# Kernel tuning notes

Hardware: AMD Instinct MI355X
Metric: run time of the kernel (lower is better)

Reference implementation:

```python
import jax, jax.numpy as jnp
import numpy as np

B, N, C = 8, 4096, 768
H = 12            # num_heads
W = 16            # window_size
S = int(N ** 0.5) # 64, token grid side
HD = C // H       # head_dim = 64
WINDOWS = (S // W) ** 2  # 16
NW = W * W               # 256 tokens per window
SCALE = HD ** -0.5


def _window_perm():
    # same ordering as the torch loop: row-major over window blocks,
    # row-major within each window
    idxs = np.arange(N).reshape(S // W, W, S // W, W)
    perm = idxs.transpose(0, 2, 1, 3).reshape(-1)
    inv_perm = np.argsort(perm)
    return jnp.asarray(perm), jnp.asarray(inv_perm)


def setup_inputs() -> dict:
    key = jax.random.key(0)
    kx, kq, kp, kb = jax.random.split(key, 4)
    x = jax.random.normal(kx, (B, N, C), dtype=jnp.float32)
    # torch nn.Linear weights: [out, in]; qkv_bias=False
    qkv_w = jax.random.normal(kq, (3 * C, C), dtype=jnp.float32) * (C ** -0.5)
    proj_w = jax.random.normal(kp, (C, C), dtype=jnp.float32) * (C ** -0.5)
    proj_b = jax.random.normal(kb, (C,), dtype=jnp.float32) * 0.02
    return {"x": x, "qkv_w": qkv_w, "proj_w": proj_w, "proj_b": proj_b}


def reference(x, qkv_w, proj_w, proj_b):
    perm, inv_perm = _window_perm()
    xp = x[:, perm]                                   # [B, N, C] window-ordered
    qkv = xp @ qkv_w.T                                # [B, N, 3C]
    qkv = qkv.reshape(B, WINDOWS, NW, 3, H, HD)
    qkv = jnp.transpose(qkv, (3, 0, 1, 4, 2, 5))      # [3, B, Wn, H, NW, HD]
    q, k, v = qkv[0], qkv[1], qkv[2]
    attn = jnp.einsum('bwhnd,bwhmd->bwhnm', q, k) * SCALE
    attn = jax.nn.softmax(attn, axis=-1)
    out = jnp.einsum('bwhnm,bwhmd->bwhnd', attn, v)   # [B, Wn, H, NW, HD]
    out = jnp.transpose(out, (0, 1, 3, 2, 4)).reshape(B, N, C)
    out = out[:, inv_perm]                            # scatter back to grid order
    return out @ proj_w.T + proj_b
```

## Files before the change

### kernel.cpp

```cpp
#include <hip/hip_runtime.h>
#include <hip/hip_bf16.h>


using short8  = __attribute__((ext_vector_type(8))) short;
using short4v = __attribute__((ext_vector_type(4))) short;
using floatx4 = __attribute__((ext_vector_type(4))) float;

#define B_    8
#define N_    4096
#define C_    768
#define H_    12
#define HD_   64
#define NW_   256
#define SCALE_ 0.125f
#define QKV_PLANE ((size_t)25165824)

__device__ __forceinline__ float bf2f(unsigned short u) {
  union { unsigned int i; float f; } c; c.i = ((unsigned int)u) << 16; return c.f;
}
__device__ __forceinline__ unsigned short f2bf(float f) {
  unsigned int u = __float_as_uint(f);
  u += 0x7fffu + ((u >> 16) & 1u);
  return (unsigned short)(u >> 16);
}
__device__ __forceinline__ short4v f4bf(floatx4 f) {
  short4v s;
  s[0] = (short)f2bf(f[0]); s[1] = (short)f2bf(f[1]);
  s[2] = (short)f2bf(f[2]); s[3] = (short)f2bf(f[3]);
  return s;
}
__device__ __forceinline__ int perm_n(int w, int t) {
  int rb = w >> 2, cb = w & 3, ri = t >> 4, ci = t & 15;
  return ((rb << 4) + ri) * 64 + (cb << 4) + ci;
}
__device__ __forceinline__ void glds16(const unsigned short* g, short* l) {
  __builtin_amdgcn_global_load_lds(
      (const __attribute__((address_space(1))) unsigned int*)g,
      (__attribute__((address_space(3))) unsigned int*)l, 16, 0, 0);
}

__global__ __launch_bounds__(192) void conv_x(
    const float* __restrict__ x, unsigned short* __restrict__ xb) {
  int row = blockIdx.x;
  int b = row >> 12, p = row & 4095;
  int n = perm_n(p >> 8, p & 255);
  const float* src = x + ((size_t)(b << 12) + (size_t)n) * C_;
  unsigned short* dst = xb + (size_t)row * C_;
  int c = threadIdx.x << 2;
  *(short4v*)(dst + c) = f4bf(*(const floatx4*)(src + c));
}

__global__ __launch_bounds__(192) void conv_w(
    const float* __restrict__ qw, const float* __restrict__ pw,
    unsigned short* __restrict__ wq, unsigned short* __restrict__ wp) {
  int row = blockIdx.x;
  const float* src; unsigned short* dst;
  if (row < 2304) { src = qw + (size_t)row * C_; dst = wq + (size_t)row * C_; }
  else { src = pw + (size_t)(row - 2304) * C_; dst = wp + (size_t)(row - 2304) * C_; }
  int c = threadIdx.x << 2;
  *(short4v*)(dst + c) = f4bf(*(const floatx4*)(src + c));
}

#define LPA 0
#define LPB 16384
#define LQA 32768
#define LQB 49152

#define STAGE8(gp, ldsbase, ksk) {                                             \
    int kc_ = (ksk) < C_ ? (ksk) : 0;                                          \
    glds16((gp) + (size_t)arow * C_ + kc_ + (sgran << 3),                      \
           L + (ldsbase) + tid * 8);                                           \
    glds16((gp) + (size_t)(arow + 64) * C_ + kc_ + (sgran << 3),               \
           L + (ldsbase) + 4096 + tid * 8);                                    \
  }

#define PH8(q, AB, BB, LOADB, STG_STMT, WV) {                                  \
    if (LOADB) {                                                               \
      _Pragma("unroll") for (int n = 0; n < 4; n++)                            \
        _Pragma("unroll") for (int kk = 0; kk < 2; kk++)                       \
          bq[n][kk] = *(const short8*)&L[(BB) + rdB + n * 1024 +               \
                                          (((kk * 4 + quad) ^ swq) << 3)];     \
    }                                                                          \
    short8 a0k0 = *(const short8*)&L[(AB) + rdA + (2*(q))*1024 +               \
                                      (((quad) ^ swq) << 3)];                  \
    short8 a0k1 = *(const short8*)&L[(AB) + rdA + (2*(q))*1024 +               \
                                      (((4 + quad) ^ swq) << 3)];              \
    short8 a1k0 = *(const short8*)&L[(AB) + rdA + (2*(q)+1)*1024 +             \
                                      (((quad) ^ swq) << 3)];                  \
    short8 a1k1 = *(const short8*)&L[(AB) + rdA + (2*(q)+1)*1024 +             \
                                      (((4 + quad) ^ swq) << 3)];              \
    STG_STMT;                                                                  \
    asm volatile("s_barrier" ::: "memory");                                    \
    asm volatile("s_waitcnt lgkmcnt(0)" ::: "memory");                         \
    __builtin_amdgcn_sched_barrier(0);                                         \
    __builtin_amdgcn_s_setprio(1);                                             \
    _Pragma("unroll") for (int n = 0; n < 4; n++) {                            \
      acc[2*(q)][n]   = __builtin_amdgcn_mfma_f32_16x16x32_bf16(               \
          a0k0, bq[n][0], acc[2*(q)][n], 0, 0, 0);                             \
      acc[2*(q)+1][n] = __builtin_amdgcn_mfma_f32_16x16x32_bf16(               \
          a1k0, bq[n][0], acc[2*(q)+1][n], 0, 0, 0);                           \
      acc[2*(q)][n]   = __builtin_amdgcn_mfma_f32_16x16x32_bf16(               \
          a0k1, bq[n][1], acc[2*(q)][n], 0, 0, 0);                             \
      acc[2*(q)+1][n] = __builtin_amdgcn_mfma_f32_16x16x32_bf16(               \
          a1k1, bq[n][1], acc[2*(q)+1][n], 0, 0, 0);                           \
    }                                                                          \
    __builtin_amdgcn_s_setprio(0);                                             \
    if (WV) { asm volatile("s_waitcnt vmcnt(4)" ::: "memory"); }               \
    asm volatile("s_barrier" ::: "memory");                                    \
  }

#define GEMM8_CORE(Aptr, Bptr)                                                 \
  __shared__ short L[65536];                                                   \
  const int tid  = threadIdx.x;                                                \
  const int bm   = blockIdx.x;                                                 \
  const int bn   = blockIdx.y;                                                 \
  const int wave = tid >> 6, lane = tid & 63;                                  \
  const int wm   = wave >> 2, wn = wave & 3;                                   \
  const int l15  = lane & 15, quad = lane >> 4;                                \
  const int swq  = l15 & 7;                                                    \
  const int sgran = (tid & 7) ^ ((tid >> 3) & 7);                              \
  const int arow  = tid >> 3;                                                  \
  const unsigned short* gA = (Aptr) + (size_t)(bm * 256) * C_;                 \
  const unsigned short* gB = (Bptr) + (size_t)(bn * 256) * C_;                 \
  const unsigned short* gA1 = gA + (size_t)128 * C_;                           \
  const unsigned short* gB1 = gB + (size_t)128 * C_;                           \
  const int rdA = wm * 8192 + l15 * 64;                                        \
  const int rdB = (wn >> 1) * 8192 + ((wn & 1) * 64 + l15) * 64;               \
  floatx4 acc[8][4];                                                           \
  short8 bq[4][2];                                                             \
  _Pragma("unroll") for (int i = 0; i < 8; i++)                                \
      _Pragma("unroll") for (int j = 0; j < 4; j++)                            \
          acc[i][j] = {0.f, 0.f, 0.f, 0.f};                                    \
                           \
  STAGE8(gA,  LPA,        0); STAGE8(gA1, LPA + 8192, 0);                      \
  STAGE8(gB,  LPB,        0); STAGE8(gB1, LPB + 8192, 0);                      \
  STAGE8(gB,  LQB,       64); STAGE8(gB1, LQB + 8192, 64);                     \
  asm volatile("s_waitcnt vmcnt(4)" ::: "memory");                             \
  asm volatile("s_barrier" ::: "memory");                                      \
  for (int it = 0; it < 6; it++) {                                             \
    const int t  = it * 2;                                                     \
    const int kA1 = (t + 1) * 64;                                              \
    const int kN2 = (t + 2) * 64;                                              \
    const int kN3 = (t + 3) * 64;                                              \
    PH8(0, LPA, LPB, 1, STAGE8(gA,  LQA,        kA1), 0)                       \
    PH8(1, LPA, LPB, 0, STAGE8(gA1, LQA + 8192, kA1), 0)                       \
    PH8(2, LPA, LPB, 0, STAGE8(gB,  LPB,        kN2), 0)                       \
    PH8(3, LPA, LPB, 0, STAGE8(gB1, LPB + 8192, kN2), 1)                       \
    PH8(0, LQA, LQB, 1, STAGE8(gA,  LPA,        kN2), 0)                       \
    PH8(1, LQA, LQB, 0, STAGE8(gA1, LPA + 8192, kN2), 0)                       \
    PH8(2, LQA, LQB, 0, STAGE8(gB,  LQB,        kN3), 0)                       \
    PH8(3, LQA, LQB, 0, STAGE8(gB1, LQB + 8192, kN3), 1)                       \
  }

__global__ __launch_bounds__(512, 2) void qkv_gemm_bf8(
    const unsigned short* __restrict__ a,
    const unsigned short* __restrict__ w,
    unsigned short* __restrict__ qkv) {
  GEMM8_CORE(a, w)
  const int which = bn / 3;
  const int jbase = (bn - which * 3) * 256;
  unsigned short* dst = qkv + (size_t)which * QKV_PLANE;
#pragma unroll
  for (int mi = 0; mi < 8; mi++) {
#pragma unroll
    for (int r = 0; r < 4; r++) {
      int mg = bm * 256 + wm * 128 + mi * 16 + quad * 4 + r;
      int b = mg >> 12, p = mg & 4095;
      int wdx = p >> 8, tt = p & 255;
      size_t base = (size_t)((b * 16 + wdx) * 12) * (NW_ * HD_) + (size_t)tt * HD_;
#pragma unroll
      for (int ni = 0; ni < 4; ni++) {
        int jj = jbase + wn * 64 + ni * 16 + l15;
        int h = jj >> 6, d = jj & 63;
        dst[base + (size_t)h * (NW_ * HD_) + d] = f2bf(acc[mi][ni][r]);
      }
    }
  }
  asm volatile("s_waitcnt vmcnt(0)" ::: "memory");
}

__global__ __launch_bounds__(512, 2) void proj_gemm_bf8(
    const unsigned short* __restrict__ a,
    const unsigned short* __restrict__ w,
    const float* __restrict__ bias,
    float* __restrict__ out) {
  GEMM8_CORE(a, w)
#pragma unroll
  for (int mi = 0; mi < 8; mi++) {
#pragma unroll
    for (int r = 0; r < 4; r++) {
      int mg = bm * 256 + wm * 128 + mi * 16 + quad * 4 + r;
      size_t rowb = (size_t)mg * C_;
#pragma unroll
      for (int ni = 0; ni < 4; ni++) {
        int jj = bn * 256 + wn * 64 + ni * 16 + l15;
        out[rowb + jj] = acc[mi][ni][r] + bias[jj];
      }
    }
  }
  asm volatile("s_waitcnt vmcnt(0)" ::: "memory");
}

__global__ __launch_bounds__(512, 2) void attn_mfma(
    const unsigned short* __restrict__ qkv,
    unsigned short* __restrict__ attn_out) {
  const int bwh = blockIdx.x;
  const int tid = threadIdx.x;
  const int wv = tid >> 6, lane = tid & 63;
  const int l15 = lane & 15, quad = lane >> 4;
  const size_t off = (size_t)bwh * (NW_ * HD_);
  const unsigned short* qb = qkv + off;
  const unsigned short* kb = qkv + QKV_PLANE + off;
  const unsigned short* vb = qkv + 2 * QKV_PLANE + off;

  __shared__ short Ks[64 * 72];
  __shared__ short Vt[64 * 72];
  __shared__ short Ps[8][16 * 72];

  short8 bq[2][2];
#pragma unroll
  for (int c = 0; c < 2; c++) {
    int mc = wv + 8 * c;
#pragma unroll
    for (int kc = 0; kc < 2; kc++)
      bq[c][kc] = *(const short8*)(qb + (mc * 16 + l15) * 64 + kc * 32 + quad * 8);
  }

  floatx4 O[2][4];
#pragma unroll
  for (int c = 0; c < 2; c++)
#pragma unroll
    for (int dt = 0; dt < 4; dt++) O[c][dt] = {0.f, 0.f, 0.f, 0.f};
  float m_run[2] = {-1e30f, -1e30f};
  float l_run[2] = {0.f, 0.f};

  const int sr = tid >> 3;
  const int sc = (tid & 7) << 3;

  for (int t = 0; t < 4; t++) {
    __syncthreads();
    {
      short8 kk8 = *(const short8*)(kb + (t * 64 + sr) * 64 + sc);
      *(short8*)&Ks[sr * 72 + sc] = kk8;
      short8 vv8 = *(const short8*)(vb + (t * 64 + sr) * 64 + sc);
#pragma unroll
      for (int j = 0; j < 8; j++) Vt[(sc + j) * 72 + sr] = vv8[j];
    }
    __syncthreads();

#pragma unroll
    for (int c = 0; c < 2; c++) {
      floatx4 st[4];
#pragma unroll
      for (int nt = 0; nt < 4; nt++) {
        short8 ak0 = *(const short8*)&Ks[(nt * 16 + l15) * 72 + quad * 8];
        short8 ak1 = *(const short8*)&Ks[(nt * 16 + l15) * 72 + 32 + quad * 8];
        floatx4 z = {0.f, 0.f, 0.f, 0.f};
        z = __builtin_amdgcn_mfma_f32_16x16x32_bf16(ak0, bq[c][0], z, 0, 0, 0);
        z = __builtin_amdgcn_mfma_f32_16x16x32_bf16(ak1, bq[c][1], z, 0, 0, 0);
        st[nt] = z;
      }
      float s[16];
      float cmax = -1e30f;
#pragma unroll
      for (int nt = 0; nt < 4; nt++)
#pragma unroll
        for (int r = 0; r < 4; r++) {
          float v = st[nt][r] * SCALE_;
          s[nt * 4 + r] = v;
          cmax = fmaxf(cmax, v);
        }
      cmax = fmaxf(cmax, __shfl_xor(cmax, 16));
      cmax = fmaxf(cmax, __shfl_xor(cmax, 32));
      float nm = fmaxf(m_run[c], cmax);
      float alpha = __expf(m_run[c] - nm);
      m_run[c] = nm;
      float psum = 0.f;
#pragma unroll
      for (int j = 0; j < 16; j++) {
        float p = __expf(s[j] - nm);
        s[j] = p;
        psum += p;
      }
      psum += __shfl_xor(psum, 16);
      psum += __shfl_xor(psum, 32);
      l_run[c] = l_run[c] * alpha + psum;
#pragma unroll
      for (int nt = 0; nt < 4; nt++) {
        short4v pv;
        pv[0] = (short)f2bf(s[nt * 4 + 0]);
        pv[1] = (short)f2bf(s[nt * 4 + 1]);
        pv[2] = (short)f2bf(s[nt * 4 + 2]);
        pv[3] = (short)f2bf(s[nt * 4 + 3]);
        *(short4v*)&Ps[wv][l15 * 72 + nt * 16 + quad * 4] = pv;
      }
      float ar[4];
#pragma unroll
      for (int r = 0; r < 4; r++) ar[r] = __shfl(alpha, quad * 4 + r);
#pragma unroll
      for (int dt = 0; dt < 4; dt++)
#pragma unroll
        for (int r = 0; r < 4; r++) O[c][dt][r] *= ar[r];
#pragma unroll
      for (int kc = 0; kc < 2; kc++) {
        short8 ap = *(const short8*)&Ps[wv][l15 * 72 + kc * 32 + quad * 8];
#pragma unroll
        for (int dt = 0; dt < 4; dt++) {
          short8 bv = *(const short8*)&Vt[(dt * 16 + l15) * 72 + kc * 32 + quad * 8];
          O[c][dt] = __builtin_amdgcn_mfma_f32_16x16x32_bf16(ap, bv, O[c][dt], 0, 0, 0);
        }
      }
    }
  }

  int h = bwh % 12, bw = bwh / 12;
  int b = bw >> 4, wdx = bw & 15;
#pragma unroll
  for (int c = 0; c < 2; c++) {
    float linv = 1.f / l_run[c];
    float lr[4];
#pragma unroll
    for (int r = 0; r < 4; r++) lr[r] = __shfl(linv, quad * 4 + r);
    int mc = wv + 8 * c;
#pragma unroll
    for (int r = 0; r < 4; r++) {
      int q = mc * 16 + quad * 4 + r;
      int n = perm_n(wdx, q);
      unsigned short* op = attn_out + ((size_t)(b * N_ + n)) * C_ + h * HD_;
#pragma unroll
      for (int dt = 0; dt < 4; dt++)
        op[dt * 16 + l15] = f2bf(O[c][dt][r] * lr[r]);
    }
  }
}

__global__ __launch_bounds__(256) void qkv_gemm_f32(
    const float* __restrict__ x,
    const float* __restrict__ w,
    unsigned short* __restrict__ qkv) {
  __shared__ short As[128 * 40];
  __shared__ short Bs[128 * 40];
  const int tid  = threadIdx.x;
  const int bm   = blockIdx.x;
  const int bn   = blockIdx.y;
  const int wave = tid >> 6, lane = tid & 63;
  const int wm   = wave >> 1, wn = wave & 1;
  const int l15  = lane & 15, quad = lane >> 4;
  const int colf  = (tid & 7) << 2;
  const int rbase = tid >> 3;
  size_t aoff[4], boff[4];
#pragma unroll
  for (int i = 0; i < 4; i++) {
    int r = rbase + 32 * i;
    int mg = bm * 128 + r;
    int b = mg >> 12, p = mg & 4095;
    int n = perm_n(p >> 8, p & 255);
    aoff[i] = ((size_t)(b << 12) + (size_t)n) * C_;
    boff[i] = (size_t)(bn * 128 + r) * C_;
  }
  floatx4 acc[4][4];
#pragma unroll
  for (int i = 0; i < 4; i++)
#pragma unroll
    for (int j = 0; j < 4; j++) acc[i][j] = {0.f, 0.f, 0.f, 0.f};
  for (int k0 = 0; k0 < C_; k0 += 32) {
#pragma unroll
    for (int i = 0; i < 4; i++) {
      int r = rbase + 32 * i;
      *(short4v*)&As[r * 40 + colf] = f4bf(*(const floatx4*)(x + aoff[i] + k0 + colf));
      *(short4v*)&Bs[r * 40 + colf] = f4bf(*(const floatx4*)(w + boff[i] + k0 + colf));
    }
    __syncthreads();
    short8 af[4], bfr[4];
#pragma unroll
    for (int mi = 0; mi < 4; mi++)
      af[mi] = *(const short8*)&As[(wm * 64 + mi * 16 + l15) * 40 + quad * 8];
#pragma unroll
    for (int ni = 0; ni < 4; ni++)
      bfr[ni] = *(const short8*)&Bs[(wn * 64 + ni * 16 + l15) * 40 + quad * 8];
#pragma unroll
    for (int mi = 0; mi < 4; mi++)
#pragma unroll
      for (int ni = 0; ni < 4; ni++)
        acc[mi][ni] = __builtin_amdgcn_mfma_f32_16x16x32_bf16(
            af[mi], bfr[ni], acc[mi][ni], 0, 0, 0);
    __syncthreads();
  }
  const int which = (bn * 128) / 768;
  const int jbase = bn * 128 - which * 768;
  unsigned short* dst = qkv + (size_t)which * QKV_PLANE;
#pragma unroll
  for (int mi = 0; mi < 4; mi++) {
#pragma unroll
    for (int r = 0; r < 4; r++) {
      int mg = bm * 128 + wm * 64 + mi * 16 + quad * 4 + r;
      int b = mg >> 12, p = mg & 4095;
      int wdx = p >> 8, t = p & 255;
      size_t base = (size_t)((b * 16 + wdx) * 12) * (NW_ * HD_) + (size_t)t * HD_;
#pragma unroll
      for (int ni = 0; ni < 4; ni++) {
        int jj = jbase + wn * 64 + ni * 16 + l15;
        int h = jj >> 6, d = jj & 63;
        dst[base + (size_t)h * (NW_ * HD_) + d] = f2bf(acc[mi][ni][r]);
      }
    }
  }
}

__global__ __launch_bounds__(256) void proj_gemm_f32(
    const unsigned short* __restrict__ a,
    const float* __restrict__ w,
    const float* __restrict__ bias,
    float* __restrict__ out) {
  __shared__ short As[128 * 40];
  __shared__ short Bs[128 * 40];
  const int tid  = threadIdx.x;
  const int bm   = blockIdx.x;
  const int bn   = blockIdx.y;
  const int wave = tid >> 6, lane = tid & 63;
  const int wm   = wave >> 1, wn = wave & 1;
  const int l15  = lane & 15, quad = lane >> 4;
  const int c0 = tid, c1 = tid + 256;
  const int r0 = c0 >> 2, kc0 = (c0 & 3) << 3;
  const int r1 = c1 >> 2, kc1 = (c1 & 3) << 3;
  const size_t a0 = (size_t)(bm * 128 + r0) * C_;
  const size_t a1 = (size_t)(bm * 128 + r1) * C_;
  const int colf  = (tid & 7) << 2;
  const int rbase = tid >> 3;
  size_t boff[4];
#pragma unroll
  for (int i = 0; i < 4; i++)
    boff[i] = (size_t)(bn * 128 + rbase + 32 * i) * C_;
  floatx4 acc[4][4];
#pragma unroll
  for (int i = 0; i < 4; i++)
#pragma unroll
    for (int j = 0; j < 4; j++) acc[i][j] = {0.f, 0.f, 0.f, 0.f};
  for (int k0 = 0; k0 < C_; k0 += 32) {
    *(short8*)&As[r0 * 40 + kc0] = *(const short8*)(a + a0 + k0 + kc0);
    *(short8*)&As[r1 * 40 + kc1] = *(const short8*)(a + a1 + k0 + kc1);
#pragma unroll
    for (int i = 0; i < 4; i++) {
      int r = rbase + 32 * i;
      *(short4v*)&Bs[r * 40 + colf] = f4bf(*(const floatx4*)(w + boff[i] + k0 + colf));
    }
    __syncthreads();
    short8 af[4], bfr[4];
#pragma unroll
    for (int mi = 0; mi < 4; mi++)
      af[mi] = *(const short8*)&As[(wm * 64 + mi * 16 + l15) * 40 + quad * 8];
#pragma unroll
    for (int ni = 0; ni < 4; ni++)
      bfr[ni] = *(const short8*)&Bs[(wn * 64 + ni * 16 + l15) * 40 + quad * 8];
#pragma unroll
    for (int mi = 0; mi < 4; mi++)
#pragma unroll
      for (int ni = 0; ni < 4; ni++)
        acc[mi][ni] = __builtin_amdgcn_mfma_f32_16x16x32_bf16(
            af[mi], bfr[ni], acc[mi][ni], 0, 0, 0);
    __syncthreads();
  }
#pragma unroll
  for (int mi = 0; mi < 4; mi++) {
#pragma unroll
    for (int r = 0; r < 4; r++) {
      int mg = bm * 128 + wm * 64 + mi * 16 + quad * 4 + r;
      size_t rowb = (size_t)mg * C_;
#pragma unroll
      for (int ni = 0; ni < 4; ni++) {
        int jj = bn * 128 + wn * 64 + ni * 16 + l15;
        out[rowb + jj] = acc[mi][ni][r] + bias[jj];
      }
    }
  }
}

extern "C" void kernel_launch(void* const* d_in, const int* in_sizes, int n_in,
                              void* d_out, int out_size, void* d_ws, size_t ws_size,
                              hipStream_t stream) {
  const float* x  = (const float*)d_in[0];
  const float* qw = (const float*)d_in[1];
  const float* pw = (const float*)d_in[2];
  const float* pb = (const float*)d_in[3];
  float* out = (float*)d_out;
  unsigned short* ws = (unsigned short*)d_ws;

  unsigned short* xb       = ws;
  unsigned short* qkv_buf  = ws + QKV_PLANE;
  unsigned short* attn_buf = ws;
  unsigned short* wb_qkv   = ws + 4 * QKV_PLANE;
  unsigned short* wb_proj  = wb_qkv + (size_t)2304 * 768;

  const size_t need = (4 * QKV_PLANE + (size_t)2304 * 768 + (size_t)768 * 768) * 2;
  if (ws_size >= need) {
    conv_x<<<dim3(B_ * N_), dim3(192), 0, stream>>>(x, xb);
    conv_w<<<dim3(3072), dim3(192), 0, stream>>>(qw, pw, wb_qkv, wb_proj);
    qkv_gemm_bf8<<<dim3(128, 9), dim3(512), 0, stream>>>(xb, wb_qkv, qkv_buf);
    attn_mfma<<<dim3(1536), dim3(512), 0, stream>>>(qkv_buf, attn_buf);
    proj_gemm_bf8<<<dim3(128, 3), dim3(512), 0, stream>>>(attn_buf, wb_proj, pb, out);
  } else {
    qkv_gemm_f32<<<dim3(256, 18), dim3(256), 0, stream>>>(x, qw, qkv_buf);
    attn_mfma<<<dim3(1536), dim3(512), 0, stream>>>(qkv_buf, attn_buf);
    proj_gemm_f32<<<dim3(256, 6), dim3(256), 0, stream>>>(attn_buf, pw, pb, out);
  }
}
```

Baseline: 439.0 us.

## Pipeline proj GEMM with 128-row tiles and double-buffer attention K/V loads

The projection GEMM moves to a custom ping-pong LDS pipeline with 128x256 tiles and doubles its grid, so 3x128 blocks become 3x256. That fills more CUs and overlaps global staging with MFMA phases under explicit barriers and priority hints. The attention kernel double-buffers K/V tiles in shared memory and prefetches the next tile into registers during compute, dropping one barrier per iteration. It also raises wave priority around the MFMA sections. The cost is more LDS per block and hand-tuned waitcnt and barrier sequencing that is fragile if the tile layout is wrong.

```diff
diff --git a/kernel.cpp b/kernel.cpp
--- a/kernel.cpp
+++ b/kernel.cpp
@@ -179,17 +179,88 @@
   asm volatile("s_waitcnt vmcnt(0)" ::: "memory");
 }
 
+#define JPA 0
+#define JPB 8192
+#define JQA 24576
+#define JQB 32768
+
+#define PH4P(q, AB, BB, LOADB, STG_STMT, WV) {                                 \
+    if (LOADB) {                                                               \
+      _Pragma("unroll") for (int n = 0; n < 4; n++)                            \
+        _Pragma("unroll") for (int kk = 0; kk < 2; kk++)                       \
+          bq[n][kk] = *(const short8*)&L[(BB) + rdB + n * 1024 +               \
+                                          (((kk * 4 + quad) ^ swq) << 3)];     \
+    }                                                                          \
+    short8 a0k0 = *(const short8*)&L[(AB) + rdA + (q)*1024 +                   \
+                                      (((quad) ^ swq) << 3)];                  \
+    short8 a0k1 = *(const short8*)&L[(AB) + rdA + (q)*1024 +                   \
+                                      (((4 + quad) ^ swq) << 3)];              \
+    STG_STMT;                                                                  \
+    asm volatile("s_barrier" ::: "memory");                                    \
+    asm volatile("s_waitcnt lgkmcnt(0)" ::: "memory");                         \
+    __builtin_amdgcn_sched_barrier(0);                                         \
+    __builtin_amdgcn_s_setprio(1);                                             \
+    _Pragma("unroll") for (int n = 0; n < 4; n++) {                            \
+      acc[q][n] = __builtin_amdgcn_mfma_f32_16x16x32_bf16(                     \
+          a0k0, bq[n][0], acc[q][n], 0, 0, 0);                                 \
+      acc[q][n] = __builtin_amdgcn_mfma_f32_16x16x32_bf16(                     \
+          a0k1, bq[n][1], acc[q][n], 0, 0, 0);                                 \
+    }                                                                          \
+    __builtin_amdgcn_s_setprio(0);                                             \
+    if (WV) { asm volatile("s_waitcnt vmcnt(4)" ::: "memory"); }               \
+    asm volatile("s_barrier" ::: "memory");                                    \
+  }
+
 __global__ __launch_bounds__(512, 2) void proj_gemm_bf8(
     const unsigned short* __restrict__ a,
     const unsigned short* __restrict__ w,
     const float* __restrict__ bias,
     float* __restrict__ out) {
-  GEMM8_CORE(a, w)
-#pragma unroll
-  for (int mi = 0; mi < 8; mi++) {
+  __shared__ short L[49152];
+  const int tid  = threadIdx.x;
+  const int bm   = blockIdx.x;
+  const int bn   = blockIdx.y;
+  const int wave = tid >> 6, lane = tid & 63;
+  const int wm   = wave >> 2, wn = wave & 3;
+  const int l15  = lane & 15, quad = lane >> 4;
+  const int swq  = l15 & 7;
+  const int sgran = (tid & 7) ^ ((tid >> 3) & 7);
+  const int arow  = tid >> 3;
+  const unsigned short* gA  = a + (size_t)(bm * 128) * C_;
+  const unsigned short* gB  = w + (size_t)(bn * 256) * C_;
+  const unsigned short* gB1 = gB + (size_t)128 * C_;
+  const int rdA = wm * 4096 + l15 * 64;
+  const int rdB = wn * 4096 + l15 * 64;
+  floatx4 acc[4][4];
+  short8 bq[4][2];
+#pragma unroll
+  for (int i = 0; i < 4; i++)
+#pragma unroll
+    for (int j = 0; j < 4; j++) acc[i][j] = {0.f, 0.f, 0.f, 0.f};
+  STAGE8(gA,  JPA,        0);
+  STAGE8(gB,  JPB,        0); STAGE8(gB1, JPB + 8192, 0);
+  STAGE8(gB,  JQB,       64); STAGE8(gB1, JQB + 8192, 64);
+  asm volatile("s_waitcnt vmcnt(4)" ::: "memory");
+  asm volatile("s_barrier" ::: "memory");
+  for (int it = 0; it < 6; it++) {
+    const int t  = it * 2;
+    const int kA1 = (t + 1) * 64;
+    const int kN2 = (t + 2) * 64;
+    const int kN3 = (t + 3) * 64;
+    PH4P(0, JPA, JPB, 1, STAGE8(gA,  JQA,        kA1), 0)
+    PH4P(1, JPA, JPB, 0, STAGE8(gB,  JPB,        kN2), 0)
+    PH4P(2, JPA, JPB, 0, STAGE8(gB1, JPB + 8192, kN2), 0)
+    PH4P(3, JPA, JPB, 0, {;}, 1)
+    PH4P(0, JQA, JQB, 1, STAGE8(gA,  JPA,        kN2), 0)
+    PH4P(1, JQA, JQB, 0, STAGE8(gB,  JQB,        kN3), 0)
+    PH4P(2, JQA, JQB, 0, STAGE8(gB1, JQB + 8192, kN3), 0)
+    PH4P(3, JQA, JQB, 0, {;}, 1)
+  }
+#pragma unroll
+  for (int mi = 0; mi < 4; mi++) {
 #pragma unroll
     for (int r = 0; r < 4; r++) {
-      int mg = bm * 256 + wm * 128 + mi * 16 + quad * 4 + r;
+      int mg = bm * 128 + wm * 64 + mi * 16 + quad * 4 + r;
       size_t rowb = (size_t)mg * C_;
 #pragma unroll
       for (int ni = 0; ni < 4; ni++) {
@@ -213,9 +284,15 @@
   const unsigned short* kb = qkv + QKV_PLANE + off;
   const unsigned short* vb = qkv + 2 * QKV_PLANE + off;
 
-  __shared__ short Ks[64 * 72];
-  __shared__ short Vt[64 * 72];
+  __shared__ short Ks[2][64 * 72];
+  __shared__ short Vt[2][64 * 72];
   __shared__ short Ps[8][16 * 72];
+
+  const int sr = tid >> 3;
+  const int sc = (tid & 7) << 3;
+
+  short8 kk = *(const short8*)(kb + sr * 64 + sc);
+  short8 vv = *(const short8*)(vb + sr * 64 + sc);
 
   short8 bq[2][2];
 #pragma unroll
@@ -234,32 +311,31 @@
   float m_run[2] = {-1e30f, -1e30f};
   float l_run[2] = {0.f, 0.f};
 
-  const int sr = tid >> 3;
-  const int sc = (tid & 7) << 3;
-
   for (int t = 0; t < 4; t++) {
-    __syncthreads();
-    {
-      short8 kk8 = *(const short8*)(kb + (t * 64 + sr) * 64 + sc);
-      *(short8*)&Ks[sr * 72 + sc] = kk8;
-      short8 vv8 = *(const short8*)(vb + (t * 64 + sr) * 64 + sc);
-#pragma unroll
-      for (int j = 0; j < 8; j++) Vt[(sc + j) * 72 + sr] = vv8[j];
+    const int buf = t & 1;
+    *(short8*)&Ks[buf][sr * 72 + sc] = kk;
+#pragma unroll
+    for (int j = 0; j < 8; j++) Vt[buf][(sc + j) * 72 + sr] = vv[j];
+    if (t < 3) {
+      kk = *(const short8*)(kb + ((t + 1) * 64 + sr) * 64 + sc);
+      vv = *(const short8*)(vb + ((t + 1) * 64 + sr) * 64 + sc);
     }
     __syncthreads();
 
 #pragma unroll
     for (int c = 0; c < 2; c++) {
       floatx4 st[4];
+      __builtin_amdgcn_s_setprio(1);
 #pragma unroll
       for (int nt = 0; nt < 4; nt++) {
-        short8 ak0 = *(const short8*)&Ks[(nt * 16 + l15) * 72 + quad * 8];
-        short8 ak1 = *(const short8*)&Ks[(nt * 16 + l15) * 72 + 32 + quad * 8];
+        short8 ak0 = *(const short8*)&Ks[buf][(nt * 16 + l15) * 72 + quad * 8];
+        short8 ak1 = *(const short8*)&Ks[buf][(nt * 16 + l15) * 72 + 32 + quad * 8];
         floatx4 z = {0.f, 0.f, 0.f, 0.f};
         z = __builtin_amdgcn_mfma_f32_16x16x32_bf16(ak0, bq[c][0], z, 0, 0, 0);
         z = __builtin_amdgcn_mfma_f32_16x16x32_bf16(ak1, bq[c][1], z, 0, 0, 0);
         st[nt] = z;
       }
+      __builtin_amdgcn_s_setprio(0);
       float s[16];
       float cmax = -1e30f;
 #pragma unroll
@@ -301,15 +377,17 @@
       for (int dt = 0; dt < 4; dt++)
 #pragma unroll
         for (int r = 0; r < 4; r++) O[c][dt][r] *= ar[r];
+      __builtin_amdgcn_s_setprio(1);
 #pragma unroll
       for (int kc = 0; kc < 2; kc++) {
         short8 ap = *(const short8*)&Ps[wv][l15 * 72 + kc * 32 + quad * 8];
 #pragma unroll
         for (int dt = 0; dt < 4; dt++) {
-          short8 bv = *(const short8*)&Vt[(dt * 16 + l15) * 72 + kc * 32 + quad * 8];
+          short8 bv = *(const short8*)&Vt[buf][(dt * 16 + l15) * 72 + kc * 32 + quad * 8];
           O[c][dt] = __builtin_amdgcn_mfma_f32_16x16x32_bf16(ap, bv, O[c][dt], 0, 0, 0);
         }
       }
+      __builtin_amdgcn_s_setprio(0);
     }
   }
 
@@ -497,7 +575,7 @@
     conv_w<<<dim3(3072), dim3(192), 0, stream>>>(qw, pw, wb_qkv, wb_proj);
     qkv_gemm_bf8<<<dim3(128, 9), dim3(512), 0, stream>>>(xb, wb_qkv, qkv_buf);
     attn_mfma<<<dim3(1536), dim3(512), 0, stream>>>(qkv_buf, attn_buf);
-    proj_gemm_bf8<<<dim3(128, 3), dim3(512), 0, stream>>>(attn_buf, wb_proj, pb, out);
+    proj_gemm_bf8<<<dim3(256, 3), dim3(512), 0, stream>>>(attn_buf, wb_proj, pb, out);
   } else {
     qkv_gemm_f32<<<dim3(256, 18), dim3(256), 0, stream>>>(x, qw, qkv_buf);
     attn_mfma<<<dim3(1536), dim3(512), 0, stream>>>(qkv_buf, attn_buf);
```

Result: faster. 424.4 us (-3.3%).
